# Kernel tuning notes

Measured on AMD Instinct MI355X. Metric: run time of the kernel, lower is better.

The kernel has to match this reference:

```python
import jax, jax.numpy as jnp
import numpy as np

NUM_HEADS = 2
HIDDEN_DIM = 128  # == node_dim
HEAD_DIM = 64     # node_dim // num_heads
NEG_SLOPE = 0.2
N_NODES = 25000
N_EDGES = 400000
NODE_DIM = 128
EDGE_DIM = 64


def setup_inputs() -> dict:
    key = jax.random.key(0)
    ks = jax.random.split(key, 16)
    s = 0.05
    return {
        "node_features": jax.random.normal(ks[0], (N_NODES, NODE_DIM), jnp.float32),
        "edge_features": jax.random.normal(ks[1], (N_EDGES, EDGE_DIM), jnp.float32),
        "edge_index": jax.random.randint(ks[2], (2, N_EDGES), 0, N_NODES, jnp.int32),
        "ni_W": jax.random.normal(ks[3], (NODE_DIM, NUM_HEADS * HIDDEN_DIM), jnp.float32) * s,
        "ni_b": jax.random.normal(ks[4], (NUM_HEADS * HIDDEN_DIM,), jnp.float32) * s,
        "nj_W": jax.random.normal(ks[5], (NODE_DIM, NUM_HEADS * HIDDEN_DIM), jnp.float32) * s,
        "nj_b": jax.random.normal(ks[6], (NUM_HEADS * HIDDEN_DIM,), jnp.float32) * s,
        "e_W": jax.random.normal(ks[7], (EDGE_DIM, NUM_HEADS * HIDDEN_DIM), jnp.float32) * s,
        "e_b": jax.random.normal(ks[8], (NUM_HEADS * HIDDEN_DIM,), jnp.float32) * s,
        "attn_proj": jax.random.normal(ks[9], (NUM_HEADS, HIDDEN_DIM), jnp.float32),
        "msg_W": jax.random.normal(ks[10], (NODE_DIM + EDGE_DIM, NODE_DIM), jnp.float32) * s,
        "msg_b": jax.random.normal(ks[11], (NODE_DIM,), jnp.float32) * s,
        "out_W": jax.random.normal(ks[12], (NODE_DIM, NODE_DIM), jnp.float32) * s,
        "out_b": jax.random.normal(ks[13], (NODE_DIM,), jnp.float32) * s,
    }


def _scatter_softmax(logits, seg, num_segments):
    # logits: [E, H], seg: [E] -> per-destination-node softmax over incident edges
    seg_max = jax.ops.segment_max(logits, seg, num_segments=num_segments)  # [N, H]
    ex = jnp.exp(logits - seg_max[seg])
    denom = jax.ops.segment_sum(ex, seg, num_segments=num_segments)  # [N, H]
    return ex / denom[seg]


def reference(node_features, edge_features, edge_index, ni_W, ni_b, nj_W, nj_b,
              e_W, e_b, attn_proj, msg_W, msg_b, out_W, out_b):
    n_nodes = node_features.shape[0]
    dst = edge_index[0]  # aggregation index (indices()[0])
    src = edge_index[1]
    ni = node_features[dst]  # [E, D]
    nj = node_features[src]  # [E, D]

    hidden = ni @ ni_W + ni_b + nj @ nj_W + nj_b + edge_features @ e_W + e_b  # [E, H*hid]
    hidden = jnp.where(hidden >= 0, hidden, NEG_SLOPE * hidden)  # LeakyReLU
    hidden = hidden.reshape(-1, NUM_HEADS, HIDDEN_DIM)

    attn_logits = jnp.einsum('ehd,hd->eh', hidden, attn_proj)  # [E, H]
    attn = _scatter_softmax(attn_logits, dst, n_nodes)  # [E, H]

    messages = jnp.concatenate((nj, edge_features), axis=-1) @ msg_W + msg_b  # [E, D]
    messages = messages.reshape(-1, NUM_HEADS, HEAD_DIM) * attn[:, :, None]
    agg = jax.ops.segment_sum(messages, dst, num_segments=n_nodes)  # [N, H, head]
    agg = agg.reshape(n_nodes, NUM_HEADS * HEAD_DIM)
    return agg @ out_W + out_b
```

## Files before the change

kernel.cpp:

```cpp
#include <hip/hip_runtime.h>

#define NEG 0.2f
typedef unsigned short u16;
typedef __bf16 bf8 __attribute__((ext_vector_type(8)));
typedef float f4 __attribute__((ext_vector_type(4)));

#define OFF_PRE   0ull
#define SZ_PRE    (25000ull*640ull)
#define OFF_BCAT  (OFF_PRE + SZ_PRE)
#define SZ_BCAT   (128ull*640ull)
#define OFF_BTOT  (OFF_BCAT + SZ_BCAT)
#define SZ_BTOT   256ull
#define OFF_LOG   (OFF_BTOT + SZ_BTOT)
#define SZ_LOG    (2ull*400000ull)
#define OFF_MAX   (OFF_LOG + SZ_LOG)
#define SZ_MAX    (2ull*25000ull)
#define OFF_DEN   (OFF_MAX + SZ_MAX)
#define SZ_DEN    (2ull*25000ull)
#define OFF_AGG   (OFF_DEN + SZ_DEN)
#define SZ_AGG    (25000ull*128ull)
#define OFF_CNT   (OFF_AGG + SZ_AGG)
#define SZ_CNT    25000ull
#define OFF_CUR   (OFF_CNT + SZ_CNT)
#define SZ_CUR    25000ull
#define OFF_PERM  (OFF_CUR + SZ_CUR)
#define SZ_PERM   400000ull
#define OFF_EWF   (OFF_PERM + SZ_PERM)
#define SZ_EWF    8192ull
#define OFF_MWF   (OFF_EWF + SZ_EWF)
#define SZ_MWF    4096ull

__device__ __forceinline__ unsigned fkey(float f) {
    unsigned u = __float_as_uint(f);
    return (u & 0x80000000u) ? ~u : (u | 0x80000000u);
}
__device__ __forceinline__ float keyf(unsigned k) {
    unsigned u = (k & 0x80000000u) ? (k & 0x7fffffffu) : ~k;
    return __uint_as_float(u);
}
__device__ __forceinline__ u16 f2b(float f) {
    unsigned u = __float_as_uint(f);
    return (u16)((u + 0x7FFFu + ((u >> 16) & 1u)) >> 16);
}
__device__ __forceinline__ bf8 pack8(float4 a, float4 b) {
    union { u16 u[8]; bf8 v; } x;
    x.u[0] = f2b(a.x); x.u[1] = f2b(a.y); x.u[2] = f2b(a.z); x.u[3] = f2b(a.w);
    x.u[4] = f2b(b.x); x.u[5] = f2b(b.y); x.u[6] = f2b(b.z); x.u[7] = f2b(b.w);
    return x.v;
}

__global__ void k_prep(const float* __restrict__ niW, const float* __restrict__ njW,
                       const float* __restrict__ msgW, const float* __restrict__ eW,
                       const float* __restrict__ nib, const float* __restrict__ njb,
                       const float* __restrict__ eb,
                       float* __restrict__ bcat, float* __restrict__ btot,
                       u16* __restrict__ ewfrag, u16* __restrict__ msgfrag) {
    int idx = blockIdx.x * 256 + threadIdx.x;
    if (idx < 128 * 640) {
        int k = idx / 640, c = idx % 640;
        float v = (c < 256) ? niW[k * 256 + c]
                : (c < 512) ? njW[k * 256 + (c - 256)]
                            : msgW[k * 128 + (c - 512)];
        bcat[idx] = v;
    }
    if (idx < 16384) {
        int c = idx >> 10, s = (idx >> 9) & 1, ln = (idx >> 3) & 63, i = idx & 7;
        int k = s * 32 + ((ln >> 4) << 3) + i;
        int col = c * 16 + (ln & 15);
        ewfrag[idx] = f2b(eW[k * 256 + col]);
    }
    if (idx < 8192) {
        int c = idx >> 10, s = (idx >> 9) & 1, ln = (idx >> 3) & 63, i = idx & 7;
        int k = s * 32 + ((ln >> 4) << 3) + i;
        int col = c * 16 + (ln & 15);
        msgfrag[idx] = f2b(msgW[(128 + k) * 128 + col]);
    }
    if (blockIdx.x == 0 && threadIdx.x < 256) {
        int c = threadIdx.x;
        btot[c] = nib[c] + njb[c] + eb[c];
    }
}

__device__ __forceinline__ void gemm_tile(const float* Al, int astride, int acol0,
                                          const float* Bl, int trow, int tcol,
                                          float acc[4][8]) {
    for (int k4 = 0; k4 < 64; k4 += 4) {
        float ar[4][4];
#pragma unroll
        for (int r = 0; r < 4; ++r)
            *(float4*)ar[r] = *(const float4*)&Al[(trow * 4 + r) * astride + acol0 + k4];
#pragma unroll
        for (int kk = 0; kk < 4; ++kk) {
            float4 b0 = *(const float4*)&Bl[(k4 + kk) * 128 + tcol * 8];
            float4 b1 = *(const float4*)&Bl[(k4 + kk) * 128 + tcol * 8 + 4];
            float bv[8] = {b0.x, b0.y, b0.z, b0.w, b1.x, b1.y, b1.z, b1.w};
#pragma unroll
            for (int r = 0; r < 4; ++r) {
                float av = ar[r][kk];
#pragma unroll
                for (int j = 0; j < 8; ++j) acc[r][j] = fmaf(av, bv[j], acc[r][j]);
            }
        }
    }
}

__global__ __launch_bounds__(256) void k_node_pre(const float* __restrict__ nf,
                                                  const float* __restrict__ bcat,
                                                  float* __restrict__ pre) {
    __shared__ float Al[64 * 128];
    __shared__ float Bl[64 * 128];
    int t = threadIdx.x, n0 = blockIdx.x * 64;
    int trow = t >> 4, tcol = t & 15;
#pragma unroll
    for (int q = 0; q < 8; ++q) {
        int g = t + 256 * q;
        int i = g >> 5, k4 = (g & 31) * 4;
        int n = n0 + i;
        float4 v = make_float4(0.f, 0.f, 0.f, 0.f);
        if (n < 25000) v = *(const float4*)&nf[(size_t)n * 128 + k4];
        *(float4*)&Al[i * 128 + k4] = v;
    }
    for (int cc = 0; cc < 5; ++cc) {
        float acc[4][8] = {};
        for (int kh = 0; kh < 2; ++kh) {
            __syncthreads();
#pragma unroll
            for (int q = 0; q < 8; ++q) {
                int g = t + 256 * q;
                int k = g >> 5, c4 = (g & 31) * 4;
                *(float4*)&Bl[k * 128 + c4] =
                    *(const float4*)&bcat[(kh * 64 + k) * 640 + cc * 128 + c4];
            }
            __syncthreads();
            gemm_tile(Al, 128, kh * 64, Bl, trow, tcol, acc);
        }
#pragma unroll
        for (int r = 0; r < 4; ++r) {
            int n = n0 + trow * 4 + r;
            if (n < 25000) {
                *(float4*)&pre[(size_t)n * 640 + cc * 128 + tcol * 8] =
                    make_float4(acc[r][0], acc[r][1], acc[r][2], acc[r][3]);
                *(float4*)&pre[(size_t)n * 640 + cc * 128 + tcol * 8 + 4] =
                    make_float4(acc[r][4], acc[r][5], acc[r][6], acc[r][7]);
            }
        }
        __syncthreads();
    }
}

__global__ void k_hist(const int* __restrict__ eidx, int* __restrict__ count) {
    int e = blockIdx.x * 256 + threadIdx.x;
    if (e < 400000) atomicAdd(&count[eidx[e]], 1);
}

__global__ __launch_bounds__(1024) void k_scan(const int* __restrict__ count,
                                               int* __restrict__ cursor) {
    __shared__ int sums[1024];
    int t = threadIdx.x;
    int base = t * 25;
    int v[25];
    int local = 0;
#pragma unroll
    for (int i = 0; i < 25; ++i) {
        int idx = base + i;
        int c = (idx < 25000) ? count[idx] : 0;
        v[i] = local;
        local += c;
    }
    sums[t] = local;
    __syncthreads();
    for (int off = 1; off < 1024; off <<= 1) {
        int x = (t >= off) ? sums[t - off] : 0;
        __syncthreads();
        sums[t] += x;
        __syncthreads();
    }
    int prefix = (t == 0) ? 0 : sums[t - 1];
#pragma unroll
    for (int i = 0; i < 25; ++i) {
        int idx = base + i;
        if (idx < 25000) cursor[idx] = prefix + v[i];
    }
}

__global__ void k_scatter(const int* __restrict__ eidx, int* __restrict__ cursor,
                          int* __restrict__ perm) {
    int e = blockIdx.x * 256 + threadIdx.x;
    if (e < 400000) {
        int d = eidx[e];
        int p = atomicAdd(&cursor[d], 1);
        perm[p] = e;
    }
}

__global__ __launch_bounds__(256) void k_edge_logits(
        const float* __restrict__ ef, const int* __restrict__ eidx,
        const u16* __restrict__ ewfrag, const float* __restrict__ pre,
        const float* __restrict__ btot, const float* __restrict__ aproj,
        float* __restrict__ logits, unsigned* __restrict__ maxkey) {
    int t = threadIdx.x;
    int w = t >> 6, l = t & 63;
    int e0 = blockIdx.x * 64 + w * 16;
    int row = l & 15, kb = l >> 4;

    const float* ap = &ef[(size_t)(e0 + row) * 64 + kb * 8];
    float4 a00 = *(const float4*)ap;
    float4 a01 = *(const float4*)(ap + 4);
    float4 a10 = *(const float4*)(ap + 32);
    float4 a11 = *(const float4*)(ap + 36);
    bf8 a0 = pack8(a00, a01), a1 = pack8(a10, a11);

    int ed[4], es[4];
#pragma unroll
    for (int r = 0; r < 4; ++r) {
        int e = e0 + kb * 4 + r;
        ed[r] = eidx[e];
        es[r] = eidx[400000 + e];
    }

    float part0[4] = {0.f, 0.f, 0.f, 0.f}, part1[4] = {0.f, 0.f, 0.f, 0.f};
#pragma unroll
    for (int c = 0; c < 16; ++c) {
        bf8 b0 = *(const bf8*)&ewfrag[(size_t)((c * 2 + 0) * 64 + l) * 8];
        bf8 b1 = *(const bf8*)&ewfrag[(size_t)((c * 2 + 1) * 64 + l) * 8];
        f4 acc = {0.f, 0.f, 0.f, 0.f};
        acc = __builtin_amdgcn_mfma_f32_16x16x32_bf16(a0, b0, acc, 0, 0, 0);
        acc = __builtin_amdgcn_mfma_f32_16x16x32_bf16(a1, b1, acc, 0, 0, 0);
        int col = c * 16 + row;
        float bt = btot[col], apj = aproj[col];
#pragma unroll
        for (int r = 0; r < 4; ++r) {
            float hid = acc[r] + pre[(size_t)ed[r] * 640 + col]
                               + pre[(size_t)es[r] * 640 + 256 + col] + bt;
            hid = hid >= 0.f ? hid : NEG * hid;
            if (c < 8) part0[r] = fmaf(hid, apj, part0[r]);
            else       part1[r] = fmaf(hid, apj, part1[r]);
        }
    }
#pragma unroll
    for (int m = 1; m < 16; m <<= 1) {
#pragma unroll
        for (int r = 0; r < 4; ++r) {
            part0[r] += __shfl_xor(part0[r], m);
            part1[r] += __shfl_xor(part1[r], m);
        }
    }
    if (row == 0) {
#pragma unroll
        for (int r = 0; r < 4; ++r) {
            int e = e0 + kb * 4 + r;
            logits[(size_t)e * 2 + 0] = part0[r];
            logits[(size_t)e * 2 + 1] = part1[r];
            atomicMax(&maxkey[ed[r] * 2 + 0], fkey(part0[r]));
            atomicMax(&maxkey[ed[r] * 2 + 1], fkey(part1[r]));
        }
    }
}

__global__ void k_soft(const int* __restrict__ eidx, float* __restrict__ logits,
                       const unsigned* __restrict__ maxkey, float* __restrict__ denom) {
    int idx = blockIdx.x * 256 + threadIdx.x;
    if (idx >= 800000) return;
    int e = idx >> 1, h = idx & 1;
    int ed = eidx[e];
    float m = keyf(maxkey[ed * 2 + h]);
    float ex = __expf(logits[idx] - m);
    logits[idx] = ex;
    atomicAdd(&denom[ed * 2 + h], ex);
}

__global__ __launch_bounds__(256) void k_messages(
        const float* __restrict__ ef, const int* __restrict__ eidx,
        const int* __restrict__ perm, const u16* __restrict__ msgfrag,
        const float* __restrict__ pre, const float* __restrict__ exbuf,
        const float* __restrict__ denom, float* __restrict__ agg) {
    __shared__ float Msg[64 * 132];
    __shared__ int dstl[64], srcl[64], eperm[64];
    __shared__ float attl[64][2];
    int t = threadIdx.x;
    int w = t >> 6, l = t & 63;
    int p0 = blockIdx.x * 64;
    int row = l & 15, kb = l >> 4;

    if (t < 64) {
        int e = perm[p0 + t];
        eperm[t] = e;
        int d = eidx[e];
        dstl[t] = d;
        srcl[t] = eidx[400000 + e];
        attl[t][0] = exbuf[(size_t)e * 2 + 0] / denom[d * 2 + 0];
        attl[t][1] = exbuf[(size_t)e * 2 + 1] / denom[d * 2 + 1];
    }
    __syncthreads();

    int ea = eperm[w * 16 + row];
    const float* apr = &ef[(size_t)ea * 64 + kb * 8];
    float4 a00 = *(const float4*)apr;
    float4 a01 = *(const float4*)(apr + 4);
    float4 a10 = *(const float4*)(apr + 32);
    float4 a11 = *(const float4*)(apr + 36);
    bf8 a0 = pack8(a00, a01), a1 = pack8(a10, a11);

    int esr[4];
    float at0[4], at1[4];
#pragma unroll
    for (int r = 0; r < 4; ++r) {
        int i4 = w * 16 + kb * 4 + r;
        esr[r] = srcl[i4];
        at0[r] = attl[i4][0];
        at1[r] = attl[i4][1];
    }

#pragma unroll
    for (int c = 0; c < 8; ++c) {
        bf8 b0 = *(const bf8*)&msgfrag[(size_t)((c * 2 + 0) * 64 + l) * 8];
        bf8 b1 = *(const bf8*)&msgfrag[(size_t)((c * 2 + 1) * 64 + l) * 8];
        f4 acc = {0.f, 0.f, 0.f, 0.f};
        acc = __builtin_amdgcn_mfma_f32_16x16x32_bf16(a0, b0, acc, 0, 0, 0);
        acc = __builtin_amdgcn_mfma_f32_16x16x32_bf16(a1, b1, acc, 0, 0, 0);
        int col = c * 16 + row;
#pragma unroll
        for (int r = 0; r < 4; ++r) {
            float m = acc[r] + pre[(size_t)esr[r] * 640 + 512 + col];
            float wm = ((c < 4) ? at0[r] : at1[r]) * m;
            Msg[(w * 16 + kb * 4 + r) * 132 + col] = wm;
        }
    }
    __syncthreads();

    int c = t & 127, half = t >> 7;
    int r0 = half * 32, r1 = r0 + 32;
    int cur = dstl[r0];
    float sum = 0.f;
    for (int r = r0; r < r1; ++r) {
        int d = dstl[r];
        if (d != cur) {
            atomicAdd(&agg[(size_t)cur * 128 + c], sum);
            sum = 0.f;
            cur = d;
        }
        sum += Msg[r * 132 + c];
    }
    atomicAdd(&agg[(size_t)cur * 128 + c], sum);
}

__global__ __launch_bounds__(256) void k_out(
        const float* __restrict__ agg, const float* __restrict__ denom,
        const float* __restrict__ msgb, const float* __restrict__ outW,
        const float* __restrict__ outb, float* __restrict__ out) {
    __shared__ float Al[64 * 128];
    __shared__ float Bl[64 * 128];
    int t = threadIdx.x, n0 = blockIdx.x * 64;
    int trow = t >> 4, tcol = t & 15;
#pragma unroll
    for (int q = 0; q < 8; ++q) {
        int g = t + 256 * q;
        int i = g >> 5, k4 = (g & 31) * 4;
        int n = n0 + i;
        float4 v = make_float4(0.f, 0.f, 0.f, 0.f);
        if (n < 25000) {
            v = *(const float4*)&agg[(size_t)n * 128 + k4];
            if (denom[n * 2 + (k4 >> 6)] > 0.f) {
                float4 mb = *(const float4*)&msgb[k4];
                v.x += mb.x; v.y += mb.y; v.z += mb.z; v.w += mb.w;
            }
        }
        *(float4*)&Al[i * 128 + k4] = v;
    }
    float acc[4][8] = {};
    for (int kh = 0; kh < 2; ++kh) {
        __syncthreads();
#pragma unroll
        for (int q = 0; q < 8; ++q) {
            int g = t + 256 * q;
            int k = g >> 5, c4 = (g & 31) * 4;
            *(float4*)&Bl[k * 128 + c4] = *(const float4*)&outW[(kh * 64 + k) * 128 + c4];
        }
        __syncthreads();
        gemm_tile(Al, 128, kh * 64, Bl, trow, tcol, acc);
    }
    float ob[8];
    *(float4*)ob = *(const float4*)&outb[tcol * 8];
    *(float4*)(ob + 4) = *(const float4*)&outb[tcol * 8 + 4];
#pragma unroll
    for (int r = 0; r < 4; ++r) {
        int n = n0 + trow * 4 + r;
        if (n < 25000) {
            *(float4*)&out[(size_t)n * 128 + tcol * 8] =
                make_float4(acc[r][0] + ob[0], acc[r][1] + ob[1], acc[r][2] + ob[2], acc[r][3] + ob[3]);
            *(float4*)&out[(size_t)n * 128 + tcol * 8 + 4] =
                make_float4(acc[r][4] + ob[4], acc[r][5] + ob[5], acc[r][6] + ob[6], acc[r][7] + ob[7]);
        }
    }
}

extern "C" void kernel_launch(void* const* d_in, const int* in_sizes, int n_in,
                              void* d_out, int out_size, void* d_ws, size_t ws_size,
                              hipStream_t stream) {
    const float* nf    = (const float*)d_in[0];
    const float* ef    = (const float*)d_in[1];
    const int*   eidx  = (const int*)d_in[2];
    const float* niW   = (const float*)d_in[3];
    const float* nib   = (const float*)d_in[4];
    const float* njW   = (const float*)d_in[5];
    const float* njb   = (const float*)d_in[6];
    const float* eW    = (const float*)d_in[7];
    const float* eb    = (const float*)d_in[8];
    const float* aproj = (const float*)d_in[9];
    const float* msgW  = (const float*)d_in[10];
    const float* msgb  = (const float*)d_in[11];
    const float* outW  = (const float*)d_in[12];
    const float* outb  = (const float*)d_in[13];

    float* ws = (float*)d_ws;
    float* pre       = ws + OFF_PRE;
    float* bcat      = ws + OFF_BCAT;
    float* btot      = ws + OFF_BTOT;
    float* logits    = ws + OFF_LOG;
    unsigned* maxkey = (unsigned*)(ws + OFF_MAX);
    float* denom     = ws + OFF_DEN;
    float* agg       = ws + OFF_AGG;
    int*   count     = (int*)(ws + OFF_CNT);
    int*   cursor    = (int*)(ws + OFF_CUR);
    int*   perm      = (int*)(ws + OFF_PERM);
    u16*   ewfrag    = (u16*)(ws + OFF_EWF);
    u16*   msgfrag   = (u16*)(ws + OFF_MWF);

    hipMemsetAsync(ws + OFF_MAX, 0, (size_t)(SZ_MAX + SZ_DEN + SZ_AGG + SZ_CNT) * 4, stream);

    k_prep<<<320, 256, 0, stream>>>(niW, njW, msgW, eW, nib, njb, eb, bcat, btot, ewfrag, msgfrag);
    k_node_pre<<<391, 256, 0, stream>>>(nf, bcat, pre);
    k_hist<<<1563, 256, 0, stream>>>(eidx, count);
    k_scan<<<1, 1024, 0, stream>>>(count, cursor);
    k_scatter<<<1563, 256, 0, stream>>>(eidx, cursor, perm);
    k_edge_logits<<<6250, 256, 0, stream>>>(ef, eidx, ewfrag, pre, btot, aproj, logits, maxkey);
    k_soft<<<3125, 256, 0, stream>>>(eidx, logits, maxkey, denom);
    k_messages<<<6250, 256, 0, stream>>>(ef, eidx, perm, msgfrag, pre, logits, denom, agg);
    k_out<<<391, 256, 0, stream>>>(agg, denom, msgb, outW, outb, (float*)d_out);
}
```

Baseline: 389.0 us.

## Store node projections in bf16 and process edges in dst-sorted order

Node pre-projections for the attention path are now stored as bf16 in a compact 512-wide array, with the message projection kept in a separate fp32 128-wide array. The scatter step writes sorted dst and src arrays, so the logits, softmax and message kernels all run in dst-sorted order and read indices contiguously. The goal is to cut gather bandwidth and improve locality for the destination-side gathers and the atomicMax/atomicAdd targets. The cost is bf16 rounding on the hidden pre-activations and extra index arrays to write.

```diff
diff --git a/kernel.cpp b/kernel.cpp
--- a/kernel.cpp
+++ b/kernel.cpp
@@ -4,10 +4,13 @@
 typedef unsigned short u16;
 typedef __bf16 bf8 __attribute__((ext_vector_type(8)));
 typedef float f4 __attribute__((ext_vector_type(4)));
-
-#define OFF_PRE   0ull
-#define SZ_PRE    (25000ull*640ull)
-#define OFF_BCAT  (OFF_PRE + SZ_PRE)
+typedef u16 u16x8 __attribute__((ext_vector_type(8)));
+
+#define OFF_PREM  0ull
+#define SZ_PREM   (25000ull*128ull)
+#define OFF_P16   (OFF_PREM + SZ_PREM)
+#define SZ_P16    (25000ull*256ull)
+#define OFF_BCAT  (OFF_P16 + SZ_P16)
 #define SZ_BCAT   (128ull*640ull)
 #define OFF_BTOT  (OFF_BCAT + SZ_BCAT)
 #define SZ_BTOT   256ull
@@ -25,7 +28,11 @@
 #define SZ_CUR    25000ull
 #define OFF_PERM  (OFF_CUR + SZ_CUR)
 #define SZ_PERM   400000ull
-#define OFF_EWF   (OFF_PERM + SZ_PERM)
+#define OFF_DST   (OFF_PERM + SZ_PERM)
+#define SZ_DST    400000ull
+#define OFF_SRC   (OFF_DST + SZ_DST)
+#define SZ_SRC    400000ull
+#define OFF_EWF   (OFF_SRC + SZ_SRC)
 #define SZ_EWF    8192ull
 #define OFF_MWF   (OFF_EWF + SZ_EWF)
 #define SZ_MWF    4096ull
@@ -41,6 +48,9 @@
 __device__ __forceinline__ u16 f2b(float f) {
     unsigned u = __float_as_uint(f);
     return (u16)((u + 0x7FFFu + ((u >> 16) & 1u)) >> 16);
+}
+__device__ __forceinline__ float b2f(u16 v) {
+    return __uint_as_float(((unsigned)v) << 16);
 }
 __device__ __forceinline__ bf8 pack8(float4 a, float4 b) {
     union { u16 u[8]; bf8 v; } x;
@@ -106,7 +116,8 @@
 
 __global__ __launch_bounds__(256) void k_node_pre(const float* __restrict__ nf,
                                                   const float* __restrict__ bcat,
-                                                  float* __restrict__ pre) {
+                                                  u16* __restrict__ pre16,
+                                                  float* __restrict__ premsg) {
     __shared__ float Al[64 * 128];
     __shared__ float Bl[64 * 128];
     int t = threadIdx.x, n0 = blockIdx.x * 64;
@@ -138,10 +149,17 @@
         for (int r = 0; r < 4; ++r) {
             int n = n0 + trow * 4 + r;
             if (n < 25000) {
-                *(float4*)&pre[(size_t)n * 640 + cc * 128 + tcol * 8] =
-                    make_float4(acc[r][0], acc[r][1], acc[r][2], acc[r][3]);
-                *(float4*)&pre[(size_t)n * 640 + cc * 128 + tcol * 8 + 4] =
-                    make_float4(acc[r][4], acc[r][5], acc[r][6], acc[r][7]);
+                if (cc < 4) {
+                    u16x8 h8;
+#pragma unroll
+                    for (int j = 0; j < 8; ++j) h8[j] = f2b(acc[r][j]);
+                    *(u16x8*)&pre16[(size_t)n * 512 + cc * 128 + tcol * 8] = h8;
+                } else {
+                    *(float4*)&premsg[(size_t)n * 128 + tcol * 8] =
+                        make_float4(acc[r][0], acc[r][1], acc[r][2], acc[r][3]);
+                    *(float4*)&premsg[(size_t)n * 128 + tcol * 8 + 4] =
+                        make_float4(acc[r][4], acc[r][5], acc[r][6], acc[r][7]);
+                }
             }
         }
         __syncthreads();
@@ -184,26 +202,39 @@
 }
 
 __global__ void k_scatter(const int* __restrict__ eidx, int* __restrict__ cursor,
-                          int* __restrict__ perm) {
+                          int* __restrict__ perm, int* __restrict__ dsts,
+                          int* __restrict__ srcs) {
     int e = blockIdx.x * 256 + threadIdx.x;
     if (e < 400000) {
         int d = eidx[e];
         int p = atomicAdd(&cursor[d], 1);
         perm[p] = e;
+        dsts[p] = d;
+        srcs[p] = eidx[400000 + e];
     }
 }
 
 __global__ __launch_bounds__(256) void k_edge_logits(
-        const float* __restrict__ ef, const int* __restrict__ eidx,
-        const u16* __restrict__ ewfrag, const float* __restrict__ pre,
+        const float* __restrict__ ef, const int* __restrict__ perm,
+        const int* __restrict__ dsts, const int* __restrict__ srcs,
+        const u16* __restrict__ ewfrag, const u16* __restrict__ pre16,
         const float* __restrict__ btot, const float* __restrict__ aproj,
-        float* __restrict__ logits, unsigned* __restrict__ maxkey) {
+        float* __restrict__ logits_s, unsigned* __restrict__ maxkey) {
+    __shared__ int eperm[64], dstl[64], srcl[64];
     int t = threadIdx.x;
     int w = t >> 6, l = t & 63;
-    int e0 = blockIdx.x * 64 + w * 16;
+    int p0 = blockIdx.x * 64;
     int row = l & 15, kb = l >> 4;
 
-    const float* ap = &ef[(size_t)(e0 + row) * 64 + kb * 8];
+    if (t < 64) {
+        eperm[t] = perm[p0 + t];
+        dstl[t] = dsts[p0 + t];
+        srcl[t] = srcs[p0 + t];
+    }
+    __syncthreads();
+
+    int ea = eperm[w * 16 + row];
+    const float* ap = &ef[(size_t)ea * 64 + kb * 8];
     float4 a00 = *(const float4*)ap;
     float4 a01 = *(const float4*)(ap + 4);
     float4 a10 = *(const float4*)(ap + 32);
@@ -213,9 +244,9 @@
     int ed[4], es[4];
 #pragma unroll
     for (int r = 0; r < 4; ++r) {
-        int e = e0 + kb * 4 + r;
-        ed[r] = eidx[e];
-        es[r] = eidx[400000 + e];
+        int i4 = w * 16 + kb * 4 + r;
+        ed[r] = dstl[i4];
+        es[r] = srcl[i4];
     }
 
     float part0[4] = {0.f, 0.f, 0.f, 0.f}, part1[4] = {0.f, 0.f, 0.f, 0.f};
@@ -230,8 +261,9 @@
         float bt = btot[col], apj = aproj[col];
 #pragma unroll
         for (int r = 0; r < 4; ++r) {
-            float hid = acc[r] + pre[(size_t)ed[r] * 640 + col]
-                               + pre[(size_t)es[r] * 640 + 256 + col] + bt;
+            float pi = b2f(pre16[(size_t)ed[r] * 512 + col]);
+            float pj = b2f(pre16[(size_t)es[r] * 512 + 256 + col]);
+            float hid = acc[r] + pi + pj + bt;
             hid = hid >= 0.f ? hid : NEG * hid;
             if (c < 8) part0[r] = fmaf(hid, apj, part0[r]);
             else       part1[r] = fmaf(hid, apj, part1[r]);
@@ -248,32 +280,33 @@
     if (row == 0) {
 #pragma unroll
         for (int r = 0; r < 4; ++r) {
-            int e = e0 + kb * 4 + r;
-            logits[(size_t)e * 2 + 0] = part0[r];
-            logits[(size_t)e * 2 + 1] = part1[r];
+            int p = p0 + w * 16 + kb * 4 + r;
+            logits_s[(size_t)p * 2 + 0] = part0[r];
+            logits_s[(size_t)p * 2 + 1] = part1[r];
             atomicMax(&maxkey[ed[r] * 2 + 0], fkey(part0[r]));
             atomicMax(&maxkey[ed[r] * 2 + 1], fkey(part1[r]));
         }
     }
 }
 
-__global__ void k_soft(const int* __restrict__ eidx, float* __restrict__ logits,
+__global__ void k_soft(const int* __restrict__ dsts, float* __restrict__ logits_s,
                        const unsigned* __restrict__ maxkey, float* __restrict__ denom) {
     int idx = blockIdx.x * 256 + threadIdx.x;
     if (idx >= 800000) return;
-    int e = idx >> 1, h = idx & 1;
-    int ed = eidx[e];
-    float m = keyf(maxkey[ed * 2 + h]);
-    float ex = __expf(logits[idx] - m);
-    logits[idx] = ex;
-    atomicAdd(&denom[ed * 2 + h], ex);
+    int p = idx >> 1, h = idx & 1;
+    int d = dsts[p];
+    float m = keyf(maxkey[d * 2 + h]);
+    float ex = __expf(logits_s[idx] - m);
+    logits_s[idx] = ex;
+    atomicAdd(&denom[d * 2 + h], ex);
 }
 
 __global__ __launch_bounds__(256) void k_messages(
-        const float* __restrict__ ef, const int* __restrict__ eidx,
-        const int* __restrict__ perm, const u16* __restrict__ msgfrag,
-        const float* __restrict__ pre, const float* __restrict__ exbuf,
-        const float* __restrict__ denom, float* __restrict__ agg) {
+        const float* __restrict__ ef, const int* __restrict__ perm,
+        const int* __restrict__ dsts, const int* __restrict__ srcs,
+        const u16* __restrict__ msgfrag, const float* __restrict__ premsg,
+        const float* __restrict__ exs, const float* __restrict__ denom,
+        float* __restrict__ agg) {
     __shared__ float Msg[64 * 132];
     __shared__ int dstl[64], srcl[64], eperm[64];
     __shared__ float attl[64][2];
@@ -283,13 +316,13 @@
     int row = l & 15, kb = l >> 4;
 
     if (t < 64) {
-        int e = perm[p0 + t];
-        eperm[t] = e;
-        int d = eidx[e];
+        int p = p0 + t;
+        eperm[t] = perm[p];
+        int d = dsts[p];
         dstl[t] = d;
-        srcl[t] = eidx[400000 + e];
-        attl[t][0] = exbuf[(size_t)e * 2 + 0] / denom[d * 2 + 0];
-        attl[t][1] = exbuf[(size_t)e * 2 + 1] / denom[d * 2 + 1];
+        srcl[t] = srcs[p];
+        attl[t][0] = exs[(size_t)p * 2 + 0] / denom[d * 2 + 0];
+        attl[t][1] = exs[(size_t)p * 2 + 1] / denom[d * 2 + 1];
     }
     __syncthreads();
 
@@ -321,7 +354,7 @@
         int col = c * 16 + row;
 #pragma unroll
         for (int r = 0; r < 4; ++r) {
-            float m = acc[r] + pre[(size_t)esr[r] * 640 + 512 + col];
+            float m = acc[r] + premsg[(size_t)esr[r] * 128 + col];
             float wm = ((c < 4) ? at0[r] : at1[r]) * m;
             Msg[(w * 16 + kb * 4 + r) * 132 + col] = wm;
         }
@@ -413,28 +446,31 @@
     const float* outb  = (const float*)d_in[13];
 
     float* ws = (float*)d_ws;
-    float* pre       = ws + OFF_PRE;
+    float* premsg    = ws + OFF_PREM;
+    u16*   pre16     = (u16*)(ws + OFF_P16);
     float* bcat      = ws + OFF_BCAT;
     float* btot      = ws + OFF_BTOT;
-    float* logits    = ws + OFF_LOG;
+    float* logits_s  = ws + OFF_LOG;
     unsigned* maxkey = (unsigned*)(ws + OFF_MAX);
     float* denom     = ws + OFF_DEN;
     float* agg       = ws + OFF_AGG;
     int*   count     = (int*)(ws + OFF_CNT);
     int*   cursor    = (int*)(ws + OFF_CUR);
     int*   perm      = (int*)(ws + OFF_PERM);
+    int*   dsts      = (int*)(ws + OFF_DST);
+    int*   srcs      = (int*)(ws + OFF_SRC);
     u16*   ewfrag    = (u16*)(ws + OFF_EWF);
     u16*   msgfrag   = (u16*)(ws + OFF_MWF);
 
     hipMemsetAsync(ws + OFF_MAX, 0, (size_t)(SZ_MAX + SZ_DEN + SZ_AGG + SZ_CNT) * 4, stream);
 
     k_prep<<<320, 256, 0, stream>>>(niW, njW, msgW, eW, nib, njb, eb, bcat, btot, ewfrag, msgfrag);
-    k_node_pre<<<391, 256, 0, stream>>>(nf, bcat, pre);
+    k_node_pre<<<391, 256, 0, stream>>>(nf, bcat, pre16, premsg);
     k_hist<<<1563, 256, 0, stream>>>(eidx, count);
     k_scan<<<1, 1024, 0, stream>>>(count, cursor);
-    k_scatter<<<1563, 256, 0, stream>>>(eidx, cursor, perm);
-    k_edge_logits<<<6250, 256, 0, stream>>>(ef, eidx, ewfrag, pre, btot, aproj, logits, maxkey);
-    k_soft<<<3125, 256, 0, stream>>>(eidx, logits, maxkey, denom);
-    k_messages<<<6250, 256, 0, stream>>>(ef, eidx, perm, msgfrag, pre, logits, denom, agg);
+    k_scatter<<<1563, 256, 0, stream>>>(eidx, cursor, perm, dsts, srcs);
+    k_edge_logits<<<6250, 256, 0, stream>>>(ef, perm, dsts, srcs, ewfrag, pre16, btot, aproj, logits_s, maxkey);
+    k_soft<<<3125, 256, 0, stream>>>(dsts, logits_s, maxkey, denom);
+    k_messages<<<6250, 256, 0, stream>>>(ef, perm, dsts, srcs, msgfrag, premsg, logits_s, denom, agg);
     k_out<<<391, 256, 0, stream>>>(agg, denom, msgb, outW, outb, (float*)d_out);
 }
```

New measurement: 364.4 us. -6.3%, faster.
